# Performance work log

Measured on AMD Instinct MI355X. Metric: run time of the kernel, lower is better.

Reference implementation:

```python
import jax, jax.numpy as jnp
import numpy as np

B, S, D_IN, H, D_OUT = 2048, 256, 3, 128, 6
DT = 0.1


def setup_inputs() -> dict:
    key = jax.random.key(0)
    ks = jax.random.split(key, 7)
    sx = 1.0 / np.sqrt(D_IN)
    sh = 1.0 / np.sqrt(H)
    return {
        "x": jax.random.normal(ks[0], (B, S, D_IN), dtype=jnp.float32),
        "W_xh": jax.random.uniform(ks[1], (H, D_IN), jnp.float32, -sx, sx),
        "W_hh": jax.random.uniform(ks[2], (H, H), jnp.float32, -sh, sh),
        "b_hh": jax.random.uniform(ks[3], (H,), jnp.float32, -sh, sh),
        "log_tau": jnp.zeros((H,), jnp.float32),
        "fc_W": jax.random.uniform(ks[4], (D_OUT, H), jnp.float32, -sh, sh),
        "fc_b": jax.random.uniform(ks[5], (D_OUT,), jnp.float32, -sh, sh),
    }


def reference(x, W_xh, W_hh, b_hh, log_tau, fc_W, fc_b):
    # tau is time-invariant: compute once outside the scan
    tau = jax.nn.softplus(log_tau) + 0.001  # [H]
    # precompute input projections for all timesteps (one big GEMM)
    xp = jnp.einsum("bsd,hd->sbh", x, W_xh)  # [S, B, H]

    def step(h, xt_proj):
        f = jnp.tanh(xt_proj + h @ W_hh.T + b_hh)  # [B, H]
        h = h + (-h + f) / tau * DT
        return h, None

    h0 = jnp.zeros((x.shape[0], W_hh.shape[0]), dtype=x.dtype)
    hT, _ = jax.lax.scan(step, h0, xp)
    params = jax.nn.softplus(hT @ fc_W.T + fc_b)  # [B, 6]
    return params
```

## Files before the change

### kernel.cpp

```cpp
#include <hip/hip_runtime.h>
#include <math.h>

#define B_TOT 2048
#define S_LEN 256
#define DIN   3
#define H     128
#define DOUT  6
#define DT_C  0.1f

#define NROWS 8
#define HPAD  136
#define PPAD  132

#define PRESCALE 2.8853900817779268f

typedef __attribute__((ext_vector_type(8))) short short8;
typedef __attribute__((ext_vector_type(4))) float f32x4;

__device__ __forceinline__ unsigned short f2bf(float f) {
  unsigned int u = __float_as_uint(f);
  u += 0x7FFFu + ((u >> 16) & 1u);
  return (unsigned short)(u >> 16);
}
__device__ __forceinline__ unsigned int pack2_bf16(float a, float b) {
  unsigned int ua = __float_as_uint(a), ub = __float_as_uint(b);
  ua = ua + 0x7FFFu + ((ua >> 16) & 1u);
  ub = ub + 0x7FFFu + ((ub >> 16) & 1u);
  return (ua >> 16) | (ub & 0xFFFF0000u);
}
__device__ __forceinline__ float dpp_xor8(float v) {
  int i = __float_as_int(v);
  int r = __builtin_amdgcn_update_dpp(i, i, 0x128 , 0xF, 0xF, false);
  return __int_as_float(r);
}

__launch_bounds__(512, 2)
__global__ void ltc_kernel(const float* __restrict__ x,
                           const float* __restrict__ W_xh,
                           const float* __restrict__ W_hh,
                           const float* __restrict__ b_hh,
                           const float* __restrict__ log_tau,
                           const float* __restrict__ fc_W,
                           const float* __restrict__ fc_b,
                           float* __restrict__ out) {
  __shared__ alignas(16) unsigned short sh_h[2][NROWS][HPAD];
  __shared__ alignas(16) float sh_p[NROWS][PPAD];

  const int tid  = threadIdx.x;
  const int w    = tid >> 6;
  const int lane = tid & 63;
  const int quad = lane >> 4;
  const int l16  = lane & 15;
  const int rb0  = blockIdx.x * NROWS;

  {
    uint4* p = (uint4*)&sh_h[0][0][0];
    const int n16 = (2 * NROWS * HPAD) / 8;
    for (int i = tid; i < n16; i += 512) p[i] = make_uint4(0, 0, 0, 0);
  }

  short8 wa[4];
  {
    const int j = w * 16 + l16;
#pragma unroll
    for (int kc = 0; kc < 4; ++kc) {
      const float* src = W_hh + j * H + kc * 32 + quad * 8;
#pragma unroll
      for (int i = 0; i < 8; ++i)
        wa[kc][i] = (short)f2bf(src[i] * PRESCALE);
    }
  }

  const int brow = l16 & 7;
  const int rbse = (l16 >> 3) * 2;
  float ewx[2][3], ebh[2], ecc[2], ea[2], encc2[2];
#pragma unroll
  for (int r = 0; r < 2; ++r) {
    const int j = w * 16 + quad * 4 + rbse + r;
    ewx[r][0] = W_xh[j * 3 + 0] * PRESCALE;
    ewx[r][1] = W_xh[j * 3 + 1] * PRESCALE;
    ewx[r][2] = W_xh[j * 3 + 2] * PRESCALE;
    ebh[r]    = b_hh[j] * PRESCALE;
    float lt  = log_tau[j];
    float tau = logf(1.f + expf(lt)) + 0.001f;
    float cc  = DT_C / tau;
    ecc[r]    = cc;
    ea[r]     = 1.f - cc;
    encc2[r]  = -2.f * cc;
  }
  const bool lowhalf = (l16 < 8);
  const float* xp = x + (size_t)(rb0 + brow) * (S_LEN * DIN);

  float hreg[2] = {0.f, 0.f};

  const int rd_off = l16 * HPAD + quad * 8;
  const int wr_off = brow * HPAD + w * 16 + quad * 4 + rbse;
  const unsigned short* __restrict__ buf0 = &sh_h[0][0][0];
  unsigned short* __restrict__ buf1 = &sh_h[1][0][0];

  short8 bf[4];
#pragma unroll
  for (int kc = 0; kc < 4; ++kc) bf[kc] = short8{0, 0, 0, 0, 0, 0, 0, 0};

  float2 pfa = *(const float2*)(xp);
  float2 pfb = *(const float2*)(xp + 2);
  float2 pfc = *(const float2*)(xp + 4);

  __syncthreads();

  auto do_step = [&](const unsigned short* __restrict__ cur,
                     unsigned short* __restrict__ nxt,
                     float xc0, float xc1, float xc2) {
    if (l16 < NROWS) {
#pragma unroll
      for (int kc = 0; kc < 4; ++kc)
        bf[kc] = *(const short8*)(cur + rd_off + kc * 32);
    }

    float t0 = __builtin_fmaf(xc2, ewx[0][2], ebh[0]);
    t0 = __builtin_fmaf(xc1, ewx[0][1], t0);
    t0 = __builtin_fmaf(xc0, ewx[0][0], t0);
    float t1 = __builtin_fmaf(xc2, ewx[1][2], ebh[1]);
    t1 = __builtin_fmaf(xc1, ewx[1][1], t1);
    t1 = __builtin_fmaf(xc0, ewx[1][0], t1);

    f32x4 ah = {0.f, 0.f, 0.f, 0.f};
#pragma unroll
    for (int kc = 0; kc < 4; ++kc)
      ah = __builtin_amdgcn_mfma_f32_16x16x32_bf16(wa[kc], bf[kc], ah, 0, 0, 0);

    float d2 = dpp_xor8(ah[2]);
    float d3 = dpp_xor8(ah[3]);
    float pre0 = lowhalf ? ah[0] : d2;
    float pre1 = lowhalf ? ah[1] : d3;

    {
      float e  = __builtin_amdgcn_exp2f(pre0 + t0);
      float rc = __builtin_amdgcn_rcpf(e + 1.f);
      hreg[0] = __builtin_fmaf(encc2[0], rc, __builtin_fmaf(hreg[0], ea[0], ecc[0]));
    }
    {
      float e  = __builtin_amdgcn_exp2f(pre1 + t1);
      float rc = __builtin_amdgcn_rcpf(e + 1.f);
      hreg[1] = __builtin_fmaf(encc2[1], rc, __builtin_fmaf(hreg[1], ea[1], ecc[1]));
    }

    *(unsigned int*)(nxt + wr_off) = pack2_bf16(hreg[0], hreg[1]);
    __syncthreads();
  };

  for (int s = 0; s < S_LEN; s += 2) {
    float2 xa = pfa, xb = pfb, xc = pfc;
    if (s + 2 < S_LEN) {
      xp += 6;
      pfa = *(const float2*)(xp);
      pfb = *(const float2*)(xp + 2);
      pfc = *(const float2*)(xp + 4);
    }
    do_step(buf0, buf1, xa.x, xa.y, xb.x);
    do_step(buf1, (unsigned short*)buf0, xb.y, xc.x, xc.y);
  }

  {
    float2 v = make_float2(hreg[0], hreg[1]);
    *(float2*)&sh_p[brow][w * 16 + quad * 4 + rbse] = v;
  }
  __syncthreads();

  if (tid < NROWS * DOUT) {
    const int b = tid / DOUT;
    const int o = tid - b * DOUT;
    const float* fw = fc_W + o * H;
    float acc = fc_b[o];
#pragma unroll 4
    for (int k = 0; k < H; ++k) acc += sh_p[b][k] * fw[k];
    float sp = (acc > 15.f) ? acc : logf(1.f + expf(acc));
    out[(rb0 + b) * DOUT + o] = sp;
  }
}

extern "C" void kernel_launch(void* const* d_in, const int* in_sizes, int n_in,
                              void* d_out, int out_size, void* d_ws, size_t ws_size,
                              hipStream_t stream) {
  const float* x       = (const float*)d_in[0];
  const float* W_xh    = (const float*)d_in[1];
  const float* W_hh    = (const float*)d_in[2];
  const float* b_hh    = (const float*)d_in[3];
  const float* log_tau = (const float*)d_in[4];
  const float* fc_W    = (const float*)d_in[5];
  const float* fc_b    = (const float*)d_in[6];
  float* out           = (float*)d_out;

  ltc_kernel<<<dim3(B_TOT / NROWS), dim3(512), 0, stream>>>(
      x, W_xh, W_hh, b_hh, log_tau, fc_W, fc_b, out);
}
```

Baseline: 145.1 us.

## Halve rows per block and waves, each wave computing two hidden tiles

```diff
diff --git a/kernel.cpp b/kernel.cpp
--- a/kernel.cpp
+++ b/kernel.cpp
@@ -8,7 +8,7 @@
 #define DOUT  6
 #define DT_C  0.1f
 
-#define NROWS 8
+#define NROWS 4
 #define HPAD  136
 #define PPAD  132
 
@@ -28,13 +28,14 @@
   ub = ub + 0x7FFFu + ((ub >> 16) & 1u);
   return (ua >> 16) | (ub & 0xFFFF0000u);
 }
-__device__ __forceinline__ float dpp_xor8(float v) {
+template <int N>
+__device__ __forceinline__ float dpp_ror(float v) {
   int i = __float_as_int(v);
-  int r = __builtin_amdgcn_update_dpp(i, i, 0x128 , 0xF, 0xF, false);
+  int r = __builtin_amdgcn_update_dpp(i, i, 0x120 | N, 0xF, 0xF, false);
   return __int_as_float(r);
 }
 
-__launch_bounds__(512, 2)
+__launch_bounds__(256, 2)
 __global__ void ltc_kernel(const float* __restrict__ x,
                            const float* __restrict__ W_xh,
                            const float* __restrict__ W_hh,
@@ -56,27 +57,31 @@
   {
     uint4* p = (uint4*)&sh_h[0][0][0];
     const int n16 = (2 * NROWS * HPAD) / 8;
-    for (int i = tid; i < n16; i += 512) p[i] = make_uint4(0, 0, 0, 0);
-  }
-
-  short8 wa[4];
-  {
-    const int j = w * 16 + l16;
+    for (int i = tid; i < n16; i += 256) p[i] = make_uint4(0, 0, 0, 0);
+  }
+
+  short8 wa[2][4];
+#pragma unroll
+  for (int t = 0; t < 2; ++t) {
+    const int j = w * 32 + t * 16 + l16;
 #pragma unroll
     for (int kc = 0; kc < 4; ++kc) {
       const float* src = W_hh + j * H + kc * 32 + quad * 8;
 #pragma unroll
       for (int i = 0; i < 8; ++i)
-        wa[kc][i] = (short)f2bf(src[i] * PRESCALE);
-    }
-  }
-
-  const int brow = l16 & 7;
-  const int rbse = (l16 >> 3) * 2;
+        wa[t][kc][i] = (short)f2bf(src[i] * PRESCALE);
+    }
+  }
+
+  const int brow = l16 & 3;
+  const int g    = l16 >> 2;
+  const int tsel = g >> 1;
+  const int rp   = g & 1;
+  const int jloc = tsel * 16 + quad * 4 + rp * 2;
   float ewx[2][3], ebh[2], ecc[2], ea[2], encc2[2];
 #pragma unroll
   for (int r = 0; r < 2; ++r) {
-    const int j = w * 16 + quad * 4 + rbse + r;
+    const int j = w * 32 + jloc + r;
     ewx[r][0] = W_xh[j * 3 + 0] * PRESCALE;
     ewx[r][1] = W_xh[j * 3 + 1] * PRESCALE;
     ewx[r][2] = W_xh[j * 3 + 2] * PRESCALE;
@@ -88,13 +93,12 @@
     ea[r]     = 1.f - cc;
     encc2[r]  = -2.f * cc;
   }
-  const bool lowhalf = (l16 < 8);
   const float* xp = x + (size_t)(rb0 + brow) * (S_LEN * DIN);
 
   float hreg[2] = {0.f, 0.f};
 
   const int rd_off = l16 * HPAD + quad * 8;
-  const int wr_off = brow * HPAD + w * 16 + quad * 4 + rbse;
+  const int wr_off = brow * HPAD + w * 32 + jloc;
   const unsigned short* __restrict__ buf0 = &sh_h[0][0][0];
   unsigned short* __restrict__ buf1 = &sh_h[1][0][0];
 
@@ -124,15 +128,22 @@
     t1 = __builtin_fmaf(xc1, ewx[1][1], t1);
     t1 = __builtin_fmaf(xc0, ewx[1][0], t1);
 
-    f32x4 ah = {0.f, 0.f, 0.f, 0.f};
-#pragma unroll
-    for (int kc = 0; kc < 4; ++kc)
-      ah = __builtin_amdgcn_mfma_f32_16x16x32_bf16(wa[kc], bf[kc], ah, 0, 0, 0);
-
-    float d2 = dpp_xor8(ah[2]);
-    float d3 = dpp_xor8(ah[3]);
-    float pre0 = lowhalf ? ah[0] : d2;
-    float pre1 = lowhalf ? ah[1] : d3;
+    f32x4 a0 = {0.f, 0.f, 0.f, 0.f};
+    f32x4 a1 = {0.f, 0.f, 0.f, 0.f};
+#pragma unroll
+    for (int kc = 0; kc < 4; ++kc) {
+      a0 = __builtin_amdgcn_mfma_f32_16x16x32_bf16(wa[0][kc], bf[kc], a0, 0, 0, 0);
+      a1 = __builtin_amdgcn_mfma_f32_16x16x32_bf16(wa[1][kc], bf[kc], a1, 0, 0, 0);
+    }
+
+    float d2 = dpp_ror<4>(a0[2]);
+    float d3 = dpp_ror<4>(a0[3]);
+    float e0 = dpp_ror<8>(a1[0]);
+    float e1 = dpp_ror<8>(a1[1]);
+    float f2 = dpp_ror<12>(a1[2]);
+    float f3 = dpp_ror<12>(a1[3]);
+    float pre0 = (g == 0) ? a0[0] : (g == 1) ? d2 : (g == 2) ? e0 : f2;
+    float pre1 = (g == 0) ? a0[1] : (g == 1) ? d3 : (g == 2) ? e1 : f3;
 
     {
       float e  = __builtin_amdgcn_exp2f(pre0 + t0);
@@ -163,7 +174,7 @@
 
   {
     float2 v = make_float2(hreg[0], hreg[1]);
-    *(float2*)&sh_p[brow][w * 16 + quad * 4 + rbse] = v;
+    *(float2*)&sh_p[brow][w * 32 + jloc] = v;
   }
   __syncthreads();
 
@@ -191,6 +202,6 @@
   const float* fc_b    = (const float*)d_in[6];
   float* out           = (float*)d_out;
 
-  ltc_kernel<<<dim3(B_TOT / NROWS), dim3(512), 0, stream>>>(
+  ltc_kernel<<<dim3(B_TOT / NROWS), dim3(256), 0, stream>>>(
       x, W_xh, W_hh, b_hh, log_tau, fc_W, fc_b, out);
 }
```

After: 162.5 us. +12.0%, slower.
